# Performance work log

Hardware: AMD Instinct MI355X
Metric: run time of the kernel (lower is better)

Reference implementation:

```python
import jax, jax.numpy as jnp
import numpy as np

WS = 8  # window size (8,8); num_token n = 64


def setup_inputs() -> dict:
    key = jax.random.key(0)
    ks = jax.random.split(key, 10)
    dim = 28        # channels c
    d = 28          # dim_head
    rank = 28       # sq_dim
    n = WS * WS     # tokens per window
    x = jax.random.normal(ks[0], (1, 8, 256, 256, dim), jnp.float32)

    def lin(k, shape, fan_in):
        return jax.random.normal(k, shape, jnp.float32) / np.sqrt(fan_in).astype(np.float32)

    return {
        "x": x,
        "W_qk": lin(ks[1], (2 * rank, dim), dim),   # to_qk (no bias)
        "W_v": lin(ks[2], (dim, dim), dim),         # to_v (no bias)
        "W_out": lin(ks[3], (dim, dim), dim),       # to_out weight
        "b_out": jnp.zeros((dim,), jnp.float32),    # to_out bias
        "W_pcq": lin(ks[4], (1, d), d),             # pc_proj_q
        "b_pcq": jnp.ones((1,), jnp.float32),       # bias_pc_proj_q (init 1.0)
        "W_pck": lin(ks[5], (1, d), d),             # pc_proj_k
        "b_pck": jnp.ones((1,), jnp.float32),
        "W_m1": lin(ks[6], (1, n), n),              # mlp1: Linear(64,1)
        "W_m2a": lin(ks[7], (n, n), n),             # mlp2: Linear(64,64)
        "W_m2b": lin(ks[8], (1, n), n),             # mlp2: Linear(64,1)
    }


def _fa_forward(x, W_qk, W_v, W_out, b_out, W_pcq, b_pcq, W_pck, b_pck, W_m1, W_m2a, W_m2b):
    b, B, H, Wd, c = x.shape
    nh, nw = H // WS, Wd // WS
    n = WS * WS
    heads = 1  # dim_head == dim == sq_dim -> heads_qk = heads_v = 1
    # window partition: 'b B (h b0) (w b1) c -> (b h w) (b0 b1) B c'
    xw = (x.reshape(b, B, nh, WS, nw, WS, c)
           .transpose(0, 2, 4, 3, 5, 1, 6)
           .reshape(b * nh * nw, n, B, c))
    qk = xw @ W_qk.T                      # [w, n, B, 2*rank]
    q, k = jnp.split(qk, 2, axis=-1)
    v = xw @ W_v.T

    def split_heads(t):                   # [w, n, B, h*d] -> [w, h, B, n, d]
        w_, n_, B_, _ = t.shape
        return t.reshape(w_, n_, B_, heads, -1).transpose(0, 3, 2, 1, 4)

    q, k, v = split_heads(q), split_heads(k), split_heads(v)

    # learned sigma per token
    sig_q = q @ W_pcq.T + b_pcq           # [w, h, B, n, 1]
    sig_k = k @ W_pck.T + b_pck
    sim = jnp.einsum('whBid,whBjd->whBij', q, k)          # raw scores
    Sigma = sig_q * jnp.swapaxes(sig_k, -1, -2)           # outer product [.., i, j]
    # diagonal removal: sim - diag_embed(diag(sim)) == zero the diagonal
    eye = jnp.eye(n, dtype=sim.dtype)
    sim_norm = sim * (1.0 - eye)
    # MLP threshold
    theta = jnp.einsum('whBij,j->whBi', sim_norm, W_m1[0])  # mlp1 over j, squeeze
    t = theta @ W_m2a.T
    t = jnp.where(t >= 0, t, 0.1 * t)                       # LeakyReLU(0.1)
    theta = (t @ W_m2b.T)[..., None]                        # [w, h, B, 1, 1]
    sim = sim * Sigma
    attn = jax.nn.softmax(sim, axis=-1) * (sim > theta).astype(sim.dtype)
    out = jnp.einsum('whBij,whBjd->whBid', attn, v)
    # merge heads: [w, h, B, n, d] -> [w, n, B, h*d]
    out = out.transpose(0, 3, 2, 1, 4).reshape(b * nh * nw, n, B, c)
    out = out @ W_out.T + b_out
    # un-window: '(b h w) (b0 b1) B c -> b B (h b0) (w b1) c'
    out = (out.reshape(b, nh, nw, WS, WS, B, c)
              .transpose(0, 5, 1, 3, 2, 4, 6)
              .reshape(b, B, H, Wd, c))
    return out


def reference(x, W_qk, W_v, W_out, b_out, W_pcq, b_pcq, W_pck, b_pck, W_m1, W_m2a, W_m2b):
    return _fa_forward(x, W_qk, W_v, W_out, b_out, W_pcq, b_pcq,
                       W_pck, b_pck, W_m1, W_m2a, W_m2b)
```

## Files before the change

kernel.cpp:

```cpp
#include <hip/hip_runtime.h>
#include <math.h>

#define C 28
#define N 64

#define A_OFF   0
#define QT_OFF  0
#define KT_OFF  1792
#define SQ_OFF  4096
#define SGK_OFF 4160
#define TH_OFF  4224
#define V_OFF   4288
#define LDS_FLOATS 6080

__global__ __launch_bounds__(128, 2)
void fa_tiled(const float* __restrict__ x,
              const float* __restrict__ Wqk,
              const float* __restrict__ Wv,
              const float* __restrict__ Wout,
              const float* __restrict__ bout,
              const float* __restrict__ Wpcq,
              const float* __restrict__ bpcq,
              const float* __restrict__ Wpck,
              const float* __restrict__ bpck,
              const float* __restrict__ Wm1,
              const float* __restrict__ Wm2a,
              const float* __restrict__ Wm2b,
              float* __restrict__ out)
{
    __shared__ float S[LDS_FLOATS];

    const int tid = threadIdx.x;
    const int wv  = tid >> 6;
    const int ln  = tid & 63;
    const int pid = blockIdx.x;
    const int win = pid >> 3;
    const int Bi  = pid & 7;
    const int hw = win >> 5, ww = win & 31;
    const int b0 = ln >> 3, b1 = ln & 7;
    const size_t base = ((((size_t)Bi * 256) + (size_t)(hw * 8 + b0)) * 256
                         + (size_t)(ww * 8 + b1)) * C;

    const int ti = tid >> 3;
    const int tj = tid & 7;
    const int rg = ti & 7;
    const int gb = ln & 56;

    {
        float xr[C];
        {
            const float4* p = (const float4*)(x + base);
            #pragma unroll
            for (int i = 0; i < 7; ++i) {
                float4 t = p[i];
                xr[4*i+0] = t.x; xr[4*i+1] = t.y; xr[4*i+2] = t.z; xr[4*i+3] = t.w;
            }
        }

        if (wv == 0) {
            float sqa0 = 0.f, sqa1 = 0.f;
            #pragma unroll 2
            for (int d4 = 0; d4 < 7; ++d4) {
                float qq[4];
                #pragma unroll
                for (int t = 0; t < 4; ++t) {
                    const int d = 4*d4 + t;
                    float a0 = 0.f, a1 = 0.f;
                    #pragma unroll
                    for (int c = 0; c < C; c += 2) {
                        a0 += Wqk[d*C + c]     * xr[c];
                        a1 += Wqk[d*C + c + 1] * xr[c+1];
                    }
                    qq[t] = a0 + a1;
                    S[QT_OFF + d*64 + ln] = qq[t];
                }
                sqa0 += qq[0] * Wpcq[4*d4+0];
                sqa1 += qq[1] * Wpcq[4*d4+1];
                sqa0 += qq[2] * Wpcq[4*d4+2];
                sqa1 += qq[3] * Wpcq[4*d4+3];
            }
            S[SQ_OFF + ln] = sqa0 + sqa1 + bpcq[0];
            #pragma unroll
            for (int d4 = 0; d4 < 4; ++d4) {
                float vv[4];
                #pragma unroll
                for (int t = 0; t < 4; ++t) {
                    const int d = 4*d4 + t;
                    float v0 = 0.f, v1 = 0.f;
                    #pragma unroll
                    for (int c = 0; c < C; c += 2) {
                        v0 += Wv[d*C + c]     * xr[c];
                        v1 += Wv[d*C + c + 1] * xr[c+1];
                    }
                    vv[t] = v0 + v1;
                }
                *(float4*)&S[V_OFF + ln*C + 4*d4] = make_float4(vv[0],vv[1],vv[2],vv[3]);
            }
        } else {
            float ak = 0.f;
            #pragma unroll 2
            for (int d4 = 0; d4 < 7; ++d4) {
                float kk[4];
                #pragma unroll
                for (int t = 0; t < 4; ++t) {
                    const int d = 4*d4 + t;
                    float k0 = 0.f, k1 = 0.f;
                    #pragma unroll
                    for (int c = 0; c < C; c += 2) {
                        k0 += Wqk[(C+d)*C + c]     * xr[c];
                        k1 += Wqk[(C+d)*C + c + 1] * xr[c+1];
                    }
                    kk[t] = k0 + k1;
                    S[KT_OFF + d*64 + ln] = kk[t];
                }
                ak += kk[0] * Wpck[4*d4+0];
                ak += kk[1] * Wpck[4*d4+1];
                ak += kk[2] * Wpck[4*d4+2];
                ak += kk[3] * Wpck[4*d4+3];
            }
            S[SGK_OFF + ln] = ak + bpck[0];
            #pragma unroll
            for (int d4 = 4; d4 < 7; ++d4) {
                float vv[4];
                #pragma unroll
                for (int t = 0; t < 4; ++t) {
                    const int d = 4*d4 + t;
                    float v0 = 0.f, v1 = 0.f;
                    #pragma unroll
                    for (int c = 0; c < C; c += 2) {
                        v0 += Wv[d*C + c]     * xr[c];
                        v1 += Wv[d*C + c + 1] * xr[c+1];
                    }
                    vv[t] = v0 + v1;
                }
                *(float4*)&S[V_OFF + ln*C + 4*d4] = make_float4(vv[0],vv[1],vv[2],vv[3]);
            }
        }
    }
    __syncthreads();

    float acc[8][4];
    #pragma unroll
    for (int cc = 0; cc < 8; ++cc)
        #pragma unroll
        for (int rr = 0; rr < 4; ++rr) acc[cc][rr] = 0.f;

    #pragma unroll 2
    for (int d = 0; d < C; ++d) {
        float4 qa = *(const float4*)&S[QT_OFF + d*64 + 4*ti];
        float4 ka = *(const float4*)&S[KT_OFF + d*64 + 8*tj];
        float4 kb = *(const float4*)&S[KT_OFF + d*64 + 8*tj + 4];
        float q4[4] = {qa.x,qa.y,qa.z,qa.w};
        float k8[8] = {ka.x,ka.y,ka.z,ka.w,kb.x,kb.y,kb.z,kb.w};
        #pragma unroll
        for (int cc = 0; cc < 8; ++cc)
            #pragma unroll
            for (int rr = 0; rr < 4; ++rr)
                acc[cc][rr] += q4[rr] * k8[cc];
    }

    {
        float4 wa = *(const float4*)&Wm1[8*tj];
        float4 wb = *(const float4*)&Wm1[8*tj + 4];
        float w8[8] = {wa.x,wa.y,wa.z,wa.w,wb.x,wb.y,wb.z,wb.w};
        const bool e0 = (4*ti == 8*tj);
        const bool e4 = (4*ti - 8*tj == 4);
        float th4[4];
        #pragma unroll
        for (int rr = 0; rr < 4; ++rr) {
            float s = 0.f;
            #pragma unroll
            for (int cc = 0; cc < 8; ++cc) {
                float term = acc[cc][rr] * w8[cc];
                if (cc == rr     && e0) term = 0.f;
                if (cc == rr + 4 && e4) term = 0.f;
                s += term;
            }
            float tot = 0.f;
            #pragma unroll
            for (int t = 0; t < 8; ++t) tot += __shfl(s, gb + t, 64);
            th4[rr] = tot;
        }
        #pragma unroll
        for (int r = 0; r < 4; ++r)
            if (tj == r) S[TH_OFF + 4*ti + r] = th4[r];
    }
    __syncthreads();

    float theta;
    {
        const float* wrow = Wm2a + ln * N;
        float a0 = 0.f, a1 = 0.f, a2 = 0.f, a3 = 0.f;
        #pragma unroll 4
        for (int i4 = 0; i4 < 16; ++i4) {
            float4 t4 = *(const float4*)&S[TH_OFF + 4*i4];
            float4 w4 = *(const float4*)&wrow[4*i4];
            a0 += t4.x*w4.x; a1 += t4.y*w4.y; a2 += t4.z*w4.z; a3 += t4.w*w4.w;
        }
        float t = (a0 + a1) + (a2 + a3);
        t = (t >= 0.f) ? t : 0.1f * t;
        theta = t * Wm2b[ln];
        #pragma unroll
        for (int off = 32; off > 0; off >>= 1)
            theta += __shfl_xor(theta, off, 64);
    }

    {
        float4 a = *(const float4*)&S[SQ_OFF + 4*ti];
        float sq4[4] = {a.x, a.y, a.z, a.w};
        float4 c0 = *(const float4*)&S[SGK_OFF + 8*tj];
        float4 c1 = *(const float4*)&S[SGK_OFF + 8*tj + 4];
        float sg8[8] = {c0.x,c0.y,c0.z,c0.w,c1.x,c1.y,c1.z,c1.w};
        #pragma unroll
        for (int cc = 0; cc < 8; ++cc)
            #pragma unroll
            for (int rr = 0; rr < 4; ++rr)
                acc[cc][rr] = (acc[cc][rr] * sq4[rr]) * sg8[cc];
    }

    float m4[4];
    #pragma unroll
    for (int rr = 0; rr < 4; ++rr) {
        float mp = -1e30f;
        #pragma unroll
        for (int cc = 0; cc < 8; ++cc) mp = fmaxf(mp, acc[cc][rr]);
        #pragma unroll
        for (int off = 1; off < 8; off <<= 1)
            mp = fmaxf(mp, __shfl_xor(mp, off, 64));
        m4[rr] = mp;
    }

    float z4[4];
    #pragma unroll
    for (int rr = 0; rr < 4; ++rr) {
        float zp = 0.f;
        #pragma unroll
        for (int cc = 0; cc < 8; ++cc) {
            float ss = acc[cc][rr];
            float e = __expf(ss - m4[rr]);
            zp += e;
            acc[cc][rr] = (ss > theta) ? e : 0.f;
        }
        float z = 0.f;
        #pragma unroll
        for (int t = 0; t < 8; ++t) z += __shfl(zp, gb + t, 64);
        z4[rr] = z;
    }

    float* Aw = &S[A_OFF + 2048*wv];
    #pragma unroll
    for (int cc = 0; cc < 8; ++cc) {
        const int j = 8*tj + cc;
        *(float4*)&Aw[j*32 + ((4*rg + 4*tj) & 31)] =
            make_float4(acc[cc][0], acc[cc][1], acc[cc][2], acc[cc][3]);
    }

    const int dg  = tj;
    const int dgc = (dg < 7) ? dg : 6;
    float pav0[4] = {0,0,0,0}, pav1[4] = {0,0,0,0};
    float pav2[4] = {0,0,0,0}, pav3[4] = {0,0,0,0};

    #pragma unroll 8
    for (int j = 0; j < 64; ++j) {
        float4 a4 = *(const float4*)&Aw[j*32 + ((4*rg + 4*(j>>3)) & 31)];
        float4 v4 = *(const float4*)&S[V_OFF + j*C + 4*dgc];
        pav0[0] += a4.x*v4.x; pav0[1] += a4.x*v4.y; pav0[2] += a4.x*v4.z; pav0[3] += a4.x*v4.w;
        pav1[0] += a4.y*v4.x; pav1[1] += a4.y*v4.y; pav1[2] += a4.y*v4.z; pav1[3] += a4.y*v4.w;
        pav2[0] += a4.z*v4.x; pav2[1] += a4.z*v4.y; pav2[2] += a4.z*v4.z; pav2[3] += a4.z*v4.w;
        pav3[0] += a4.w*v4.x; pav3[1] += a4.w*v4.y; pav3[2] += a4.w*v4.z; pav3[3] += a4.w*v4.w;
    }

    {
        float rz0 = 1.0f / z4[0], rz1 = 1.0f / z4[1];
        float rz2 = 1.0f / z4[2], rz3 = 1.0f / z4[3];
        #pragma unroll
        for (int t = 0; t < 4; ++t) {
            pav0[t] *= rz0; pav1[t] *= rz1; pav2[t] *= rz2; pav3[t] *= rz3;
        }
    }

    if (dg < 7) {
        *(float4*)&Aw[(4*rg+0)*C + 4*dg] = make_float4(pav0[0],pav0[1],pav0[2],pav0[3]);
        *(float4*)&Aw[(4*rg+1)*C + 4*dg] = make_float4(pav1[0],pav1[1],pav1[2],pav1[3]);
        *(float4*)&Aw[(4*rg+2)*C + 4*dg] = make_float4(pav2[0],pav2[1],pav2[2],pav2[3]);
        *(float4*)&Aw[(4*rg+3)*C + 4*dg] = make_float4(pav3[0],pav3[1],pav3[2],pav3[3]);
    }
    __syncthreads();

    float o[C];
    {
        const float* orow = &S[A_OFF + 2048*(ln >> 5) + (ln & 31)*C];
        #pragma unroll
        for (int i = 0; i < 7; ++i) {
            float4 t = *(const float4*)(orow + 4*i);
            o[4*i+0] = t.x; o[4*i+1] = t.y; o[4*i+2] = t.z; o[4*i+3] = t.w;
        }
    }
    if (wv == 0) {
        float y[16];
        #pragma unroll 2
        for (int e4 = 0; e4 < 4; ++e4) {
            #pragma unroll
            for (int t = 0; t < 4; ++t) {
                const int e = 4*e4 + t;
                float a0 = 0.f, a1 = 0.f;
                #pragma unroll
                for (int d = 0; d < C; d += 2) {
                    a0 += Wout[e*C + d]     * o[d];
                    a1 += Wout[e*C + d + 1] * o[d+1];
                }
                y[e] = (a0 + a1) + bout[e];
            }
        }
        float4* yp = (float4*)(out + base);
        #pragma unroll
        for (int i = 0; i < 4; ++i)
            yp[i] = make_float4(y[4*i+0], y[4*i+1], y[4*i+2], y[4*i+3]);
    } else {
        float y[12];
        #pragma unroll 2
        for (int e4 = 0; e4 < 3; ++e4) {
            #pragma unroll
            for (int t = 0; t < 4; ++t) {
                const int e = 16 + 4*e4 + t;
                float a0 = 0.f, a1 = 0.f;
                #pragma unroll
                for (int d = 0; d < C; d += 2) {
                    a0 += Wout[e*C + d]     * o[d];
                    a1 += Wout[e*C + d + 1] * o[d+1];
                }
                y[4*e4+t] = (a0 + a1) + bout[e];
            }
        }
        float4* yp = (float4*)(out + base + 16);
        #pragma unroll
        for (int i = 0; i < 3; ++i)
            yp[i] = make_float4(y[4*i+0], y[4*i+1], y[4*i+2], y[4*i+3]);
    }
}

extern "C" void kernel_launch(void* const* d_in, const int* in_sizes, int n_in,
                              void* d_out, int out_size, void* d_ws, size_t ws_size,
                              hipStream_t stream) {
    const float* x     = (const float*)d_in[0];
    const float* W_qk  = (const float*)d_in[1];
    const float* W_v   = (const float*)d_in[2];
    const float* W_out = (const float*)d_in[3];
    const float* b_out = (const float*)d_in[4];
    const float* W_pcq = (const float*)d_in[5];
    const float* b_pcq = (const float*)d_in[6];
    const float* W_pck = (const float*)d_in[7];
    const float* b_pck = (const float*)d_in[8];
    const float* W_m1  = (const float*)d_in[9];
    const float* W_m2a = (const float*)d_in[10];
    const float* W_m2b = (const float*)d_in[11];
    float* y = (float*)d_out;

    hipLaunchKernelGGL(fa_tiled, dim3(8192), dim3(128), 0, stream,
                       x, W_qk, W_v, W_out, b_out, W_pcq, b_pcq,
                       W_pck, b_pck, W_m1, W_m2a, W_m2b, y);
}
```

Baseline: 227.2 us.

## Shrink LDS footprint by deferring V stores and splitting attention tile in halves

Holds the V projection in registers until the Q/K tiles in shared memory are no longer needed, then stores it into the freed region. The per-wave attention buffer is halved by writing and consuming the 64 key columns as two 32-column chunks. Total shared memory per block drops from about 24KB to 16KB, which is meant to let more blocks reside per CU. The cost is extra registers for the held V values, one added barrier, and two passes over the PV loop.

```diff
diff --git a/kernel.cpp b/kernel.cpp
--- a/kernel.cpp
+++ b/kernel.cpp
@@ -7,11 +7,11 @@
 #define A_OFF   0
 #define QT_OFF  0
 #define KT_OFF  1792
-#define SQ_OFF  4096
-#define SGK_OFF 4160
-#define TH_OFF  4224
-#define V_OFF   4288
-#define LDS_FLOATS 6080
+#define V_OFF   2048
+#define SQ_OFF  3840
+#define SGK_OFF 3904
+#define TH_OFF  3968
+#define LDS_FLOATS 4032
 
 __global__ __launch_bounds__(128, 2)
 void fa_tiled(const float* __restrict__ x,
@@ -46,6 +46,8 @@
     const int rg = ti & 7;
     const int gb = ln & 56;
 
+    float vv[16];
+
     {
         float xr[C];
         {
@@ -82,7 +84,6 @@
             S[SQ_OFF + ln] = sqa0 + sqa1 + bpcq[0];
             #pragma unroll
             for (int d4 = 0; d4 < 4; ++d4) {
-                float vv[4];
                 #pragma unroll
                 for (int t = 0; t < 4; ++t) {
                     const int d = 4*d4 + t;
@@ -92,9 +93,8 @@
                         v0 += Wv[d*C + c]     * xr[c];
                         v1 += Wv[d*C + c + 1] * xr[c+1];
                     }
-                    vv[t] = v0 + v1;
-                }
-                *(float4*)&S[V_OFF + ln*C + 4*d4] = make_float4(vv[0],vv[1],vv[2],vv[3]);
+                    vv[4*d4+t] = v0 + v1;
+                }
             }
         } else {
             float ak = 0.f;
@@ -121,7 +121,6 @@
             S[SGK_OFF + ln] = ak + bpck[0];
             #pragma unroll
             for (int d4 = 4; d4 < 7; ++d4) {
-                float vv[4];
                 #pragma unroll
                 for (int t = 0; t < 4; ++t) {
                     const int d = 4*d4 + t;
@@ -131,9 +130,8 @@
                         v0 += Wv[d*C + c]     * xr[c];
                         v1 += Wv[d*C + c + 1] * xr[c+1];
                     }
-                    vv[t] = v0 + v1;
-                }
-                *(float4*)&S[V_OFF + ln*C + 4*d4] = make_float4(vv[0],vv[1],vv[2],vv[3]);
+                    vv[4*(d4-4)+t] = v0 + v1;
+                }
             }
         }
     }
@@ -187,6 +185,17 @@
     }
     __syncthreads();
 
+    if (wv == 0) {
+        *(float4*)&S[V_OFF + ln*C +  0] = make_float4(vv[0], vv[1], vv[2], vv[3]);
+        *(float4*)&S[V_OFF + ln*C +  4] = make_float4(vv[4], vv[5], vv[6], vv[7]);
+        *(float4*)&S[V_OFF + ln*C +  8] = make_float4(vv[8], vv[9], vv[10],vv[11]);
+        *(float4*)&S[V_OFF + ln*C + 12] = make_float4(vv[12],vv[13],vv[14],vv[15]);
+    } else {
+        *(float4*)&S[V_OFF + ln*C + 16] = make_float4(vv[0], vv[1], vv[2], vv[3]);
+        *(float4*)&S[V_OFF + ln*C + 20] = make_float4(vv[4], vv[5], vv[6], vv[7]);
+        *(float4*)&S[V_OFF + ln*C + 24] = make_float4(vv[8], vv[9], vv[10],vv[11]);
+    }
+
     float theta;
     {
         const float* wrow = Wm2a + ln * N;
@@ -247,13 +256,16 @@
         z4[rr] = z;
     }
 
-    float* Aw = &S[A_OFF + 2048*wv];
-    #pragma unroll
-    for (int cc = 0; cc < 8; ++cc) {
-        const int j = 8*tj + cc;
-        *(float4*)&Aw[j*32 + ((4*rg + 4*tj) & 31)] =
-            make_float4(acc[cc][0], acc[cc][1], acc[cc][2], acc[cc][3]);
-    }
+    float* Aw = &S[A_OFF + 1024*wv];
+    if ((tj >> 2) == 0) {
+        #pragma unroll
+        for (int cc = 0; cc < 8; ++cc) {
+            const int jl = 8*(tj & 3) + cc;
+            *(float4*)&Aw[jl*32 + ((4*rg + 4*(jl & 7)) & 31)] =
+                make_float4(acc[cc][0], acc[cc][1], acc[cc][2], acc[cc][3]);
+        }
+    }
+    __syncthreads();
 
     const int dg  = tj;
     const int dgc = (dg < 7) ? dg : 6;
@@ -261,9 +273,28 @@
     float pav2[4] = {0,0,0,0}, pav3[4] = {0,0,0,0};
 
     #pragma unroll 8
-    for (int j = 0; j < 64; ++j) {
-        float4 a4 = *(const float4*)&Aw[j*32 + ((4*rg + 4*(j>>3)) & 31)];
-        float4 v4 = *(const float4*)&S[V_OFF + j*C + 4*dgc];
+    for (int jl = 0; jl < 32; ++jl) {
+        float4 a4 = *(const float4*)&Aw[jl*32 + ((4*rg + 4*(jl & 7)) & 31)];
+        float4 v4 = *(const float4*)&S[V_OFF + jl*C + 4*dgc];
+        pav0[0] += a4.x*v4.x; pav0[1] += a4.x*v4.y; pav0[2] += a4.x*v4.z; pav0[3] += a4.x*v4.w;
+        pav1[0] += a4.y*v4.x; pav1[1] += a4.y*v4.y; pav1[2] += a4.y*v4.z; pav1[3] += a4.y*v4.w;
+        pav2[0] += a4.z*v4.x; pav2[1] += a4.z*v4.y; pav2[2] += a4.z*v4.z; pav2[3] += a4.z*v4.w;
+        pav3[0] += a4.w*v4.x; pav3[1] += a4.w*v4.y; pav3[2] += a4.w*v4.z; pav3[3] += a4.w*v4.w;
+    }
+
+    if ((tj >> 2) == 1) {
+        #pragma unroll
+        for (int cc = 0; cc < 8; ++cc) {
+            const int jl = 8*(tj & 3) + cc;
+            *(float4*)&Aw[jl*32 + ((4*rg + 4*(jl & 7)) & 31)] =
+                make_float4(acc[cc][0], acc[cc][1], acc[cc][2], acc[cc][3]);
+        }
+    }
+
+    #pragma unroll 8
+    for (int jl = 0; jl < 32; ++jl) {
+        float4 a4 = *(const float4*)&Aw[jl*32 + ((4*rg + 4*(jl & 7)) & 31)];
+        float4 v4 = *(const float4*)&S[V_OFF + (32 + jl)*C + 4*dgc];
         pav0[0] += a4.x*v4.x; pav0[1] += a4.x*v4.y; pav0[2] += a4.x*v4.z; pav0[3] += a4.x*v4.w;
         pav1[0] += a4.y*v4.x; pav1[1] += a4.y*v4.y; pav1[2] += a4.y*v4.z; pav1[3] += a4.y*v4.w;
         pav2[0] += a4.z*v4.x; pav2[1] += a4.z*v4.y; pav2[2] += a4.z*v4.z; pav2[3] += a4.z*v4.w;
@@ -289,7 +320,7 @@
 
     float o[C];
     {
-        const float* orow = &S[A_OFF + 2048*(ln >> 5) + (ln & 31)*C];
+        const float* orow = &S[A_OFF + 1024*(ln >> 5) + (ln & 31)*C];
         #pragma unroll
         for (int i = 0; i < 7; ++i) {
             float4 t = *(const float4*)(orow + 4*i);
```

Result: no change. 228.6 us (+0.6%).
